# Optimization experiments

Measured on AMD Instinct MI355X. Metric: run time of the kernel, lower is better.

Reference implementation:

```python
import jax, jax.numpy as jnp
import numpy as np
from jax import lax

B, C, H, W = 8, 256, 128, 128
O = 256
KH, KW = 1, 3
PH, PW = 0, 1
K = KH * KW


def setup_inputs() -> dict:
    key = jax.random.key(0)
    k1, k2, k3, k4 = jax.random.split(key, 4)
    x = jax.random.normal(k1, (B, C, H, W), jnp.float32)
    # offset-predicting conv (small init so sample points stay near the grid)
    offset_w = jax.random.normal(k2, (2 * K, C, KH, KW), jnp.float32) * 0.01
    offset_b = jax.random.normal(k3, (2 * K,), jnp.float32) * 0.01
    # deformable conv weight, no bias (bias=False in the module)
    deform_w = jax.random.normal(k4, (O, C, KH, KW), jnp.float32) * (1.0 / np.sqrt(C * K))
    return {"x": x, "offset_w": offset_w, "offset_b": offset_b, "deform_w": deform_w}


def _gather_corner(x_flat, yi, xi, valid_dtype):
    # x_flat: [B, C, H*W]; yi, xi: int32 [B, K, Ho, Wo]
    valid = (yi >= 0) & (yi < H) & (xi >= 0) & (xi < W)
    yc = jnp.clip(yi, 0, H - 1)
    xc = jnp.clip(xi, 0, W - 1)
    idx = yc * W + xc  # [B, K, Ho, Wo]
    # per-batch fancy gather -> [B, C, K, Ho, Wo]
    g = jax.vmap(lambda f, i: f[:, i])(x_flat, idx)
    return g * valid[:, None].astype(valid_dtype)


def _deform_conv(x, offset, deform_w):
    # torchvision-style deform_conv2d with zero padding, groups=1, dg=1
    Ho, Wo = offset.shape[2], offset.shape[3]
    off = offset.reshape(B, K, 2, Ho, Wo)
    off_y, off_x = off[:, :, 0], off[:, :, 1]  # [B, K, Ho, Wo]

    k = jnp.arange(K)
    base_y = (-PH + (k // KW)).astype(x.dtype)[None, :, None, None]
    base_x = (-PW + (k % KW)).astype(x.dtype)[None, :, None, None]
    grid_y = jnp.arange(Ho, dtype=x.dtype)[None, None, :, None]
    grid_x = jnp.arange(Wo, dtype=x.dtype)[None, None, None, :]

    py = grid_y + base_y + off_y  # fractional sample rows [B,K,Ho,Wo]
    px = grid_x + base_x + off_x  # fractional sample cols

    y0f = jnp.floor(py)
    x0f = jnp.floor(px)
    wy = (py - y0f)[:, None]  # [B,1,K,Ho,Wo]
    wx = (px - x0f)[:, None]
    y0 = y0f.astype(jnp.int32)
    x0 = x0f.astype(jnp.int32)
    y1 = y0 + 1
    x1 = x0 + 1

    x_flat = x.reshape(B, C, H * W)
    v00 = _gather_corner(x_flat, y0, x0, x.dtype)
    v01 = _gather_corner(x_flat, y0, x1, x.dtype)
    v10 = _gather_corner(x_flat, y1, x0, x.dtype)
    v11 = _gather_corner(x_flat, y1, x1, x.dtype)

    sampled = (v00 * (1 - wy) * (1 - wx) + v01 * (1 - wy) * wx
               + v10 * wy * (1 - wx) + v11 * wy * wx)  # [B,C,K,Ho,Wo]

    return jnp.einsum('bckhw,ock->bohw', sampled, deform_w.reshape(O, C, K))


def reference(x, offset_w, offset_b, deform_w):
    # offset conv (stride 1, padding (0,1))
    offset = lax.conv_general_dilated(x, offset_w, window_strides=(1, 1),
                                      padding=[(PH, PH), (PW, PW)])
    offset = offset + offset_b[None, :, None, None]
    # in-place zeroing from the original forward
    offset = offset.at[:, 1].set(0.0).at[:, 4].set(0.0)
    return _deform_conv(x, offset, deform_w)
```

## Files before the change

### kernel.cpp

```cpp
#include <hip/hip_runtime.h>
#include <hip/hip_bf16.h>
#include <hip/hip_fp16.h>

#define Bn 8
#define Cn 256
#define Hn 128
#define Wn 128
#define On 256
#define HWn (Hn*Wn)
#define Pn  HWn
#define W2ROW 768
#define QC  ((size_t)Pn * Cn)

typedef __attribute__((ext_vector_type(8))) short bf16x8;
typedef __attribute__((ext_vector_type(4))) float f32x4;

__device__ __forceinline__ void gload_lds16(const void* g, void* l) {
  __builtin_amdgcn_global_load_lds(
      (__attribute__((address_space(1))) void*)g,
      (__attribute__((address_space(3))) void*)l, 16, 0, 0);
}

__device__ __forceinline__ unsigned short f2bf(float f) {
  unsigned int u = __float_as_uint(f);
  unsigned int r = (u + 0x7fffu + ((u >> 16) & 1u)) >> 16;
  return (unsigned short)r;
}
__device__ __forceinline__ float bf2f(unsigned short u) {
  return __uint_as_float(((unsigned int)u) << 16);
}
__device__ __forceinline__ float h2f(unsigned int u16) {
  return __half2float(__ushort_as_half((unsigned short)u16));
}
__device__ __forceinline__ void bacc(uint4 v, float w, float* f) {
  f[0] += w * __uint_as_float(v.x << 16);
  f[1] += w * __uint_as_float(v.x & 0xffff0000u);
  f[2] += w * __uint_as_float(v.y << 16);
  f[3] += w * __uint_as_float(v.y & 0xffff0000u);
  f[4] += w * __uint_as_float(v.z << 16);
  f[5] += w * __uint_as_float(v.z & 0xffff0000u);
  f[6] += w * __uint_as_float(v.w << 16);
  f[7] += w * __uint_as_float(v.w & 0xffff0000u);
}

__global__ __launch_bounds__(256) void k_wprep(
    const float* __restrict__ dw, const float* __restrict__ ow,
    unsigned short* __restrict__ W2, unsigned short* __restrict__ Woff) {
  int r = blockIdx.x;
  int c = threadIdx.x;
  if (r < 768) {
    int k = r >> 8, o = r & 255;
    W2[(size_t)o * W2ROW + k * 256 + c] = f2bf(dw[((size_t)o * Cn + c) * 3 + k]);
  } else {
    int rr = r - 768;
    float v = 0.f;
    if (rr < 18) { int oc = rr / 3, kw = rr - 3 * oc; v = ow[((size_t)oc * Cn + c) * 3 + kw]; }
    Woff[(size_t)rr * Cn + c] = f2bf(v);
  }
}

__global__ __launch_bounds__(256) void k_transpose(
    const float* __restrict__ x, unsigned short* __restrict__ xbT) {
  int b = blockIdx.z;
  int q0 = blockIdx.x * 64, c0 = blockIdx.y * 64;
  __shared__ unsigned short t[64][66];
  int tid = threadIdx.x;
  int qq = (tid & 15) * 4;
  int cb = tid >> 4;
  const float* xb = x + (size_t)b * Cn * HWn;
  #pragma unroll
  for (int i = 0; i < 4; ++i) {
    int cl = cb + 16 * i;
    float4 v = *(const float4*)(xb + (size_t)(c0 + cl) * HWn + q0 + qq);
    unsigned lo = (unsigned)f2bf(v.x) | ((unsigned)f2bf(v.y) << 16);
    unsigned hi = (unsigned)f2bf(v.z) | ((unsigned)f2bf(v.w) << 16);
    *(unsigned*)&t[cl][qq]     = lo;
    *(unsigned*)&t[cl][qq + 2] = hi;
  }
  __syncthreads();
  unsigned short* dst = xbT + (size_t)b * QC;
  int c2 = (tid & 31) * 2, qg = tid >> 5;
  #pragma unroll
  for (int j = 0; j < 8; ++j) {
    int ql = j * 8 + qg;
    unsigned int u = (unsigned int)t[c2][ql] | ((unsigned int)t[c2 + 1][ql] << 16);
    *(unsigned int*)(dst + (size_t)(q0 + ql) * Cn + c0 + c2) = u;
  }
}

__global__ __launch_bounds__(512) void k_fgemm(
    const unsigned short* __restrict__ xbT,
    const unsigned short* __restrict__ W2,
    const unsigned short* __restrict__ Woff,
    const float* __restrict__ obias,
    float* __restrict__ out) {
  int pt = blockIdx.x, z = blockIdx.y;
  int ho = (pt & 7) * 16 + (pt >> 3);
  const unsigned short* xz = xbT + (size_t)z * QC;

  __shared__ unsigned short Qs[256 * 64];
  __shared__ unsigned short Ss[128 * 64];
  __shared__ unsigned short Goff_lds[128][32];
  __shared__ unsigned int Sqb[128][3];
  __shared__ unsigned int Swh[128][3][2];

  int tid = threadIdx.x;
  int lane = tid & 63, wid = tid >> 6;
  int lg = lane >> 4;
  int q0p = ho * Wn;

  {
    f32x4 aco0 = (f32x4){0.f, 0.f, 0.f, 0.f};
    f32x4 aco1 = (f32x4){0.f, 0.f, 0.f, 0.f};
    for (int kt = 0; kt < 4; ++kt) {
      int ck0 = kt * 64;
      __syncthreads();
      #pragma unroll
      for (int i = 0; i < 2; ++i) {
        int t = tid + i * 512;
        int fo = t << 4;
        int row = fo >> 7, slot = (fo >> 4) & 7, ss2 = slot ^ (row & 7);
        gload_lds16(xz + (size_t)(q0p + row) * Cn + ck0 + ss2 * 8, (char*)Qs + fo);
      }
      if (tid < 256) {
        int fo = tid << 4;
        int row = fo >> 7, slot = (fo >> 4) & 7, ss2 = slot ^ (row & 7);
        gload_lds16(Woff + (size_t)row * Cn + ck0 + ss2 * 8, (char*)Ss + fo);
      }
      __syncthreads();
      #pragma unroll
      for (int s = 0; s < 2; ++s) {
        int arow = wid * 16 + (lane & 15);
        int aslot = (s * 4 + lg) ^ (arow & 7);
        bf16x8 af = *(const bf16x8*)((const char*)Qs + arow * 128 + aslot * 16);
        int brow0 = (lane & 15);
        int bslot0 = (s * 4 + lg) ^ (brow0 & 7);
        bf16x8 bf0 = *(const bf16x8*)((const char*)Ss + brow0 * 128 + bslot0 * 16);
        aco0 = __builtin_amdgcn_mfma_f32_16x16x32_bf16(af, bf0, aco0, 0, 0, 0);
        int brow1 = 16 + (lane & 15);
        int bslot1 = (s * 4 + lg) ^ (brow1 & 7);
        bf16x8 bf1 = *(const bf16x8*)((const char*)Ss + brow1 * 128 + bslot1 * 16);
        aco1 = __builtin_amdgcn_mfma_f32_16x16x32_bf16(af, bf1, aco1, 0, 0, 0);
      }
    }
    #pragma unroll
    for (int rr = 0; rr < 4; ++rr) {
      int qrow = wid * 16 + lg * 4 + rr;
      Goff_lds[qrow][(lane & 15)]      = f2bf(aco0[rr]);
      Goff_lds[qrow][16 + (lane & 15)] = f2bf(aco1[rr]);
    }
  }
  __syncthreads();

  if (tid < 384) {
    int k = tid >> 7;
    int wo = tid & 127;
    float offy = 0.f, offx = 0.f;
    int ocy = 2 * k, ocx = 2 * k + 1;
    if (ocy != 4) {
      float s = obias[ocy];
      #pragma unroll
      for (int kw = 0; kw < 3; ++kw) {
        int col = wo + kw - 1;
        if (col >= 0 && col < Wn)
          s += bf2f(Goff_lds[col][ocy * 3 + kw]);
      }
      offy = s;
    }
    if (ocx != 1) {
      float s = obias[ocx];
      #pragma unroll
      for (int kw = 0; kw < 3; ++kw) {
        int col = wo + kw - 1;
        if (col >= 0 && col < Wn)
          s += bf2f(Goff_lds[col][ocx * 3 + kw]);
      }
      offx = s;
    }
    float py = (float)ho + offy;
    float px = (float)(wo + k - 1) + offx;
    float y0f = floorf(py), x0f = floorf(px);
    float wy = py - y0f, wx = px - x0f;
    int y0 = (int)y0f, x0 = (int)x0f;
    int y1 = y0 + 1, x1 = x0 + 1;
    bool vy0 = (y0 >= 0) && (y0 < Hn), vy1 = (y1 >= 0) && (y1 < Hn);
    bool vx0 = (x0 >= 0) && (x0 < Wn), vx1 = (x1 >= 0) && (x1 < Wn);
    int yc0 = min(max(y0, 0), Hn - 1), yc1 = min(max(y1, 0), Hn - 1);
    int xc0 = min(max(x0, 0), Wn - 1), xc1 = min(max(x1, 0), Wn - 1);
    float w00 = (vy0 && vx0) ? (1.f - wy) * (1.f - wx) : 0.f;
    float w01 = (vy0 && vx1) ? (1.f - wy) * wx : 0.f;
    float w10 = (vy1 && vx0) ? wy * (1.f - wx) : 0.f;
    float w11 = (vy1 && vx1) ? wy * wx : 0.f;
    Sqb[wo][k] = (unsigned)yc0 | ((unsigned)xc0 << 8) | ((unsigned)yc1 << 16) | ((unsigned)xc1 << 24);
    unsigned short h00 = __half_as_ushort(__float2half_rn(w00));
    unsigned short h01 = __half_as_ushort(__float2half_rn(w01));
    unsigned short h10 = __half_as_ushort(__float2half_rn(w10));
    unsigned short h11 = __half_as_ushort(__float2half_rn(w11));
    Swh[wo][k][0] = (unsigned)h00 | ((unsigned)h01 << 16);
    Swh[wo][k][1] = (unsigned)h10 | ((unsigned)h11 << 16);
  }

  int wr = wid >> 1, wc = wid & 1;
  int oct = tid & 7, pg = tid >> 3;
  int plA = pg, plB = pg + 64;
  f32x4 acc[4][4];
  #pragma unroll
  for (int m = 0; m < 4; ++m)
    #pragma unroll
    for (int n = 0; n < 4; ++n) acc[m][n] = (f32x4){0.f, 0.f, 0.f, 0.f};

  __syncthreads();

  const char* xzb = (const char*)xz;
  int octo = oct * 16;
  int dsA = plA * 128 + ((oct ^ (plA & 7)) << 4);
  int dsB = plB * 128 + ((oct ^ (plB & 7)) << 4);

  uint4 gA0, gA1, gA2, gA3, gB0, gB1, gB2, gB3;
  unsigned wpa0, wpa1, wpb0, wpb1;

  #define PREF(KT) do {                                                        \
    int kk = (KT) >> 2;                                                        \
    const char* bse = xzb + (((KT) & 3) << 7) + octo;                          \
    unsigned qpA = Sqb[plA][kk], qpB = Sqb[plB][kk];                           \
    wpa0 = Swh[plA][kk][0]; wpa1 = Swh[plA][kk][1];                            \
    wpb0 = Swh[plB][kk][0]; wpb1 = Swh[plB][kk][1];                            \
    int yA0 = (int)(qpA & 255u) << 16, xA0 = (int)((qpA >> 8) & 255u) << 9;    \
    int yA1 = (int)((qpA >> 16) & 255u) << 16, xA1 = (int)(qpA >> 24) << 9;    \
    int yB0 = (int)(qpB & 255u) << 16, xB0 = (int)((qpB >> 8) & 255u) << 9;    \
    int yB1 = (int)((qpB >> 16) & 255u) << 16, xB1 = (int)(qpB >> 24) << 9;    \
    gA0 = *(const uint4*)(bse + yA0 + xA0);                                    \
    gA1 = *(const uint4*)(bse + yA0 + xA1);                                    \
    gA2 = *(const uint4*)(bse + yA1 + xA0);                                    \
    gA3 = *(const uint4*)(bse + yA1 + xA1);                                    \
    gB0 = *(const uint4*)(bse + yB0 + xB0);                                    \
    gB1 = *(const uint4*)(bse + yB0 + xB1);                                    \
    gB2 = *(const uint4*)(bse + yB1 + xB0);                                    \
    gB3 = *(const uint4*)(bse + yB1 + xB1);                                    \
  } while (0)

  PREF(0);

  #pragma unroll
  for (int kt = 0; kt < 12; ++kt) {
    int k = kt >> 2;
    int c0 = (kt & 3) << 6;
    __syncthreads();
    #pragma unroll
    for (int i = 0; i < 4; ++i) {
      int t = tid + i * 512;
      int fo = t << 4;
      int row = fo >> 7;
      int slot = (fo >> 4) & 7;
      int ss = slot ^ (row & 7);
      gload_lds16(W2 + (size_t)row * W2ROW + k * 256 + c0 + ss * 8, (char*)Qs + fo);
    }
    {
      float f[8] = {0.f, 0.f, 0.f, 0.f, 0.f, 0.f, 0.f, 0.f};
      bacc(gA0, h2f(wpa0 & 0xffffu), f); bacc(gA1, h2f(wpa0 >> 16), f);
      bacc(gA2, h2f(wpa1 & 0xffffu), f); bacc(gA3, h2f(wpa1 >> 16), f);
      uint4 r;
      r.x = (unsigned)f2bf(f[0]) | ((unsigned)f2bf(f[1]) << 16);
      r.y = (unsigned)f2bf(f[2]) | ((unsigned)f2bf(f[3]) << 16);
      r.z = (unsigned)f2bf(f[4]) | ((unsigned)f2bf(f[5]) << 16);
      r.w = (unsigned)f2bf(f[6]) | ((unsigned)f2bf(f[7]) << 16);
      *(uint4*)((char*)Ss + dsA) = r;
    }
    {
      float f[8] = {0.f, 0.f, 0.f, 0.f, 0.f, 0.f, 0.f, 0.f};
      bacc(gB0, h2f(wpb0 & 0xffffu), f); bacc(gB1, h2f(wpb0 >> 16), f);
      bacc(gB2, h2f(wpb1 & 0xffffu), f); bacc(gB3, h2f(wpb1 >> 16), f);
      uint4 r;
      r.x = (unsigned)f2bf(f[0]) | ((unsigned)f2bf(f[1]) << 16);
      r.y = (unsigned)f2bf(f[2]) | ((unsigned)f2bf(f[3]) << 16);
      r.z = (unsigned)f2bf(f[4]) | ((unsigned)f2bf(f[5]) << 16);
      r.w = (unsigned)f2bf(f[6]) | ((unsigned)f2bf(f[7]) << 16);
      *(uint4*)((char*)Ss + dsB) = r;
    }
    __syncthreads();
    if (kt < 11) PREF(kt + 1);
    #pragma unroll
    for (int s = 0; s < 2; ++s) {
      bf16x8 af[4], bfr[4];
      #pragma unroll
      for (int m = 0; m < 4; ++m) {
        int row = wr * 64 + m * 16 + (lane & 15);
        int slot = (s * 4 + lg) ^ (row & 7);
        af[m] = *(const bf16x8*)((const char*)Qs + row * 128 + slot * 16);
      }
      #pragma unroll
      for (int n = 0; n < 4; ++n) {
        int row = wc * 64 + n * 16 + (lane & 15);
        int slot = (s * 4 + lg) ^ (row & 7);
        bfr[n] = *(const bf16x8*)((const char*)Ss + row * 128 + slot * 16);
      }
      #pragma unroll
      for (int m = 0; m < 4; ++m)
        #pragma unroll
        for (int n = 0; n < 4; ++n)
          acc[m][n] = __builtin_amdgcn_mfma_f32_16x16x32_bf16(af[m], bfr[n], acc[m][n], 0, 0, 0);
    }
  }
  #undef PREF

  float* ob_ = out + (size_t)z * On * Pn + (size_t)ho * Wn;
  #pragma unroll
  for (int m = 0; m < 4; ++m)
    #pragma unroll
    for (int n = 0; n < 4; ++n)
      #pragma unroll
      for (int rr = 0; rr < 4; ++rr) {
        int o = wr * 64 + m * 16 + lg * 4 + rr;
        int pc = wc * 64 + n * 16 + (lane & 15);
        ob_[(size_t)o * Pn + pc] = acc[m][n][rr];
      }
}

extern "C" void kernel_launch(void* const* d_in, const int* in_sizes, int n_in,
                              void* d_out, int out_size, void* d_ws, size_t ws_size,
                              hipStream_t stream) {
  const float* x  = (const float*)d_in[0];
  const float* ow = (const float*)d_in[1];
  const float* ob = (const float*)d_in[2];
  const float* dw = (const float*)d_in[3];
  float* out = (float*)d_out;

  char* ws = (char*)d_ws;
  size_t w2_bytes   = (size_t)On * W2ROW * 2;
  size_t woff_bytes = (size_t)32 * Cn * 2;
  size_t xbT_bytes  = QC * 2;
  size_t w2_al   = (w2_bytes + 255) & ~(size_t)255;
  size_t woff_al = (woff_bytes + 255) & ~(size_t)255;

  unsigned short* W2   = (unsigned short*)ws;
  unsigned short* Woff = (unsigned short*)(ws + w2_al);
  unsigned short* xbT  = (unsigned short*)(ws + w2_al + woff_al);
  (void)ws_size; (void)xbT_bytes;

  k_wprep<<<800, 256, 0, stream>>>(dw, ow, W2, Woff);
  k_transpose<<<dim3(256, 4, Bn), 256, 0, stream>>>(x, xbT);
  k_fgemm<<<dim3(128, Bn), 512, 0, stream>>>(xbT, W2, Woff, ob, out);
}
```

Measured before the change: 169.1 us.

## Overlap transpose of next batches with GEMM of previous batches in mixed launches

Replaces the separate transpose and fused-GEMM kernels with one mixed kernel launched five times. Each launch runs the GEMM blocks for two batches and the transpose blocks for the next two batches, so memory-bound transpose work can overlap compute-bound GEMM work. The transpose tile grows to cover all 256 channels per block with 512 threads, and shared memory becomes one raw buffer carved by offset. This adds extra launch overhead and a larger shared-memory footprint for transpose blocks, and the Goff_lds row pitch changes from 32 to 34 (padding).

```diff
diff --git a/kernel.cpp b/kernel.cpp
--- a/kernel.cpp
+++ b/kernel.cpp
@@ -59,52 +59,59 @@
   }
 }
 
-__global__ __launch_bounds__(256) void k_transpose(
-    const float* __restrict__ x, unsigned short* __restrict__ xbT) {
-  int b = blockIdx.z;
-  int q0 = blockIdx.x * 64, c0 = blockIdx.y * 64;
-  __shared__ unsigned short t[64][66];
-  int tid = threadIdx.x;
-  int qq = (tid & 15) * 4;
-  int cb = tid >> 4;
-  const float* xb = x + (size_t)b * Cn * HWn;
-  #pragma unroll
-  for (int i = 0; i < 4; ++i) {
-    int cl = cb + 16 * i;
-    float4 v = *(const float4*)(xb + (size_t)(c0 + cl) * HWn + q0 + qq);
-    unsigned lo = (unsigned)f2bf(v.x) | ((unsigned)f2bf(v.y) << 16);
-    unsigned hi = (unsigned)f2bf(v.z) | ((unsigned)f2bf(v.w) << 16);
-    *(unsigned*)&t[cl][qq]     = lo;
-    *(unsigned*)&t[cl][qq + 2] = hi;
-  }
-  __syncthreads();
-  unsigned short* dst = xbT + (size_t)b * QC;
-  int c2 = (tid & 31) * 2, qg = tid >> 5;
-  #pragma unroll
-  for (int j = 0; j < 8; ++j) {
-    int ql = j * 8 + qg;
-    unsigned int u = (unsigned int)t[c2][ql] | ((unsigned int)t[c2 + 1][ql] << 16);
-    *(unsigned int*)(dst + (size_t)(q0 + ql) * Cn + c0 + c2) = u;
-  }
-}
-
-__global__ __launch_bounds__(512) void k_fgemm(
-    const unsigned short* __restrict__ xbT,
+__global__ __launch_bounds__(512) void k_mix(
+    const float* __restrict__ x,
+    unsigned short* __restrict__ xbT,
     const unsigned short* __restrict__ W2,
     const unsigned short* __restrict__ Woff,
     const float* __restrict__ obias,
-    float* __restrict__ out) {
-  int pt = blockIdx.x, z = blockIdx.y;
+    float* __restrict__ out,
+    int bF0, int nbF, int bT0) {
+  __shared__ __attribute__((aligned(16))) char smem[62464];
+  int tid = threadIdx.x;
+  int nf = nbF << 7;
+
+  if ((int)blockIdx.x >= nf) {
+    int tix = blockIdx.x - nf;
+    int b = bT0 + (tix >> 8);
+    int q0 = (tix & 255) * 64;
+    unsigned short (*t)[66] = (unsigned short (*)[66])smem;
+    int qq = (tid & 15) * 4;
+    int cb = tid >> 4;
+    const float* xb = x + (size_t)b * Cn * HWn;
+    #pragma unroll
+    for (int i = 0; i < 8; ++i) {
+      int cl = cb + 32 * i;
+      float4 v = *(const float4*)(xb + (size_t)cl * HWn + q0 + qq);
+      unsigned lo = (unsigned)f2bf(v.x) | ((unsigned)f2bf(v.y) << 16);
+      unsigned hi = (unsigned)f2bf(v.z) | ((unsigned)f2bf(v.w) << 16);
+      *(unsigned*)&t[cl][qq]     = lo;
+      *(unsigned*)&t[cl][qq + 2] = hi;
+    }
+    __syncthreads();
+    unsigned short* dst = xbT + (size_t)b * QC + (size_t)q0 * Cn;
+    int c2 = (tid & 127) * 2, qg = tid >> 7;
+    #pragma unroll
+    for (int j = 0; j < 16; ++j) {
+      int ql = j * 4 + qg;
+      unsigned u = (unsigned)t[c2][ql] | ((unsigned)t[c2 + 1][ql] << 16);
+      *(unsigned*)(dst + (size_t)ql * Cn + c2) = u;
+    }
+    return;
+  }
+
+  int idx = blockIdx.x;
+  int z = bF0 + (idx >> 7);
+  int pt = idx & 127;
   int ho = (pt & 7) * 16 + (pt >> 3);
   const unsigned short* xz = xbT + (size_t)z * QC;
 
-  __shared__ unsigned short Qs[256 * 64];
-  __shared__ unsigned short Ss[128 * 64];
-  __shared__ unsigned short Goff_lds[128][32];
-  __shared__ unsigned int Sqb[128][3];
-  __shared__ unsigned int Swh[128][3][2];
-
-  int tid = threadIdx.x;
+  unsigned short* Qs = (unsigned short*)smem;
+  unsigned short* Ss = (unsigned short*)(smem + 32768);
+  unsigned short (*Goff_lds)[34] = (unsigned short (*)[34])(smem + 49152);
+  unsigned int (*Sqb)[3]    = (unsigned int (*)[3])(smem + 57856);
+  unsigned int (*Swh)[3][2] = (unsigned int (*)[3][2])(smem + 59392);
+
   int lane = tid & 63, wid = tid >> 6;
   int lg = lane >> 4;
   int q0p = ho * Wn;
@@ -117,8 +124,8 @@
       __syncthreads();
       #pragma unroll
       for (int i = 0; i < 2; ++i) {
-        int t = tid + i * 512;
-        int fo = t << 4;
+        int t2 = tid + i * 512;
+        int fo = t2 << 4;
         int row = fo >> 7, slot = (fo >> 4) & 7, ss2 = slot ^ (row & 7);
         gload_lds16(xz + (size_t)(q0p + row) * Cn + ck0 + ss2 * 8, (char*)Qs + fo);
       }
@@ -248,8 +255,8 @@
     __syncthreads();
     #pragma unroll
     for (int i = 0; i < 4; ++i) {
-      int t = tid + i * 512;
-      int fo = t << 4;
+      int t2 = tid + i * 512;
+      int fo = t2 << 4;
       int row = fo >> 7;
       int slot = (fo >> 4) & 7;
       int ss = slot ^ (row & 7);
@@ -328,16 +335,21 @@
   char* ws = (char*)d_ws;
   size_t w2_bytes   = (size_t)On * W2ROW * 2;
   size_t woff_bytes = (size_t)32 * Cn * 2;
-  size_t xbT_bytes  = QC * 2;
   size_t w2_al   = (w2_bytes + 255) & ~(size_t)255;
   size_t woff_al = (woff_bytes + 255) & ~(size_t)255;
 
   unsigned short* W2   = (unsigned short*)ws;
   unsigned short* Woff = (unsigned short*)(ws + w2_al);
   unsigned short* xbT  = (unsigned short*)(ws + w2_al + woff_al);
-  (void)ws_size; (void)xbT_bytes;
+  (void)ws_size;
 
   k_wprep<<<800, 256, 0, stream>>>(dw, ow, W2, Woff);
-  k_transpose<<<dim3(256, 4, Bn), 256, 0, stream>>>(x, xbT);
-  k_fgemm<<<dim3(128, Bn), 512, 0, stream>>>(xbT, W2, Woff, ob, out);
-}
+  for (int s = 0; s <= 4; ++s) {
+    int nbF = (s >= 1) ? 2 : 0;
+    int bF0 = (s - 1) * 2;
+    int nbT = (s <= 3) ? 2 : 0;
+    int bT0 = s * 2;
+    int grid = nbF * 128 + nbT * 256;
+    k_mix<<<grid, 512, 0, stream>>>(x, xbT, W2, Woff, ob, out, bF0, nbF, bT0);
+  }
+}
```

Result: slower. 184.7 us (+9.3%).
